# Kernel optimization log

Hardware: AMD Instinct MI355X
Metric: run time of the kernel (lower is better)

Reference implementation:

```python
import jax, jax.numpy as jnp
import numpy as np

N, T, C, K = 32, 1024, 512, 64
EPS = 1e-12  # torch F.normalize eps


def _l2norm(v, axis):
    n = jnp.sqrt(jnp.sum(v * v, axis=axis, keepdims=True))
    return v / jnp.maximum(n, EPS)


def setup_inputs() -> dict:
    key = jax.random.key(0)
    k1, k2 = jax.random.split(key)
    x = jax.random.normal(k1, (N, T, C), dtype=jnp.float32)
    centroids = jax.random.uniform(k2, (K, C), dtype=jnp.float32)
    # mirrors _init_params: conv.weight = 0.2*centroids, conv.bias = -0.1*||centroids||
    W = 0.2 * centroids
    b = -0.1 * jnp.sqrt(jnp.sum(centroids * centroids, axis=1))
    return {"x": x, "W": W, "b": b, "centroids": centroids}


def reference(x, W, b, centroids):
    # x: [N, T, C] -> [N, C, T]
    xt = jnp.transpose(x, (0, 2, 1))
    # 1x1 Conv1d == per-timestep linear: logits [N, K, T]
    logits = jnp.einsum('kc,nct->nkt', W, xt) + b[None, :, None]
    a = jax.nn.softmax(logits, axis=1)  # softmax over clusters
    # vlad[n,k,c] = sum_t a[n,k,t] * (x[n,c,t] - centroid[k,c])
    #            = (a @ x^T) - sum_t(a) * centroid  (GEMM form, same math)
    vlad = jnp.einsum('nkt,nct->nkc', a, xt) - a.sum(axis=-1)[:, :, None] * centroids[None]
    vlad = _l2norm(vlad, axis=2)          # intra-normalization per cluster
    vlad = vlad.reshape(vlad.shape[0], -1)
    vlad = _l2norm(vlad, axis=1)          # global L2 normalization
    return vlad
```

## Files before the change

### kernel.cpp

```cpp
#include <hip/hip_runtime.h>
#include <cmath>

namespace {

constexpr int N = 32, T = 1024, C = 512, K = 64;
constexpr float EPS = 1e-12f;

typedef short s8v __attribute__((ext_vector_type(8)));
typedef short s4v __attribute__((ext_vector_type(4)));
typedef float f4v __attribute__((ext_vector_type(4)));

__device__ inline unsigned short f2bh(float f) {
  __bf16 h = (__bf16)f;
  return __builtin_bit_cast(unsigned short, h);
}
__device__ inline float bh2f(unsigned short u) {
  __bf16 h = __builtin_bit_cast(__bf16, u);
  return (float)h;
}

#define MFMA16(A, B, Cc) __builtin_amdgcn_mfma_f32_16x16x32_bf16((A), (B), (Cc), 0, 0, 0)

__global__ __launch_bounds__(512, 4) void k_gemm1(
    const float* __restrict__ x, const float* __restrict__ W,
    const float* __restrict__ b, float* __restrict__ aT,
    float* __restrict__ asum_part) {
  __shared__ __align__(16) unsigned short sm[4 * 64 * 72];
  __shared__ float asum_l[512];
  unsigned short* xh_s = sm;
  unsigned short* xl_s = sm + 64 * 72;
  unsigned short* wh_s = sm + 2 * 64 * 72;
  unsigned short* wl_s = sm + 3 * 64 * 72;

  const int tid = threadIdx.x;
  const int w = tid >> 6, lane = tid & 63, lm = lane & 15, lq = lane >> 4;
  const int th = w >> 2;
  const int kq = w & 3;
  const long r0 = (long)blockIdx.x * 64;
  const int n = blockIdx.x >> 4, tl = blockIdx.x & 15;

  f4v acc[2] = {};
  float4 px[2], pw[2];
#pragma unroll
  for (int r = 0; r < 2; ++r) {
    const int f = tid + r * 512, t = f >> 4, cg = f & 15;
    px[r] = *(const float4*)&x[(r0 + t) * C + cg * 4];
    pw[r] = *(const float4*)&W[(long)t * C + cg * 4];
  }

  for (int c0 = 0; c0 < C; c0 += 64) {
    __syncthreads();
#pragma unroll
    for (int r = 0; r < 2; ++r) {
      const int f = tid + r * 512, t = f >> 4, cg = f & 15;
      const float ex[4] = {px[r].x, px[r].y, px[r].z, px[r].w};
      const float ew[4] = {pw[r].x, pw[r].y, pw[r].z, pw[r].w};
      s4v xh, xl, wh, wl;
#pragma unroll
      for (int i = 0; i < 4; ++i) {
        unsigned short hb = f2bh(ex[i]);
        xh[i] = (short)hb; xl[i] = (short)f2bh(ex[i] - bh2f(hb));
        hb = f2bh(ew[i]);
        wh[i] = (short)hb; wl[i] = (short)f2bh(ew[i] - bh2f(hb));
      }
      *(s4v*)&xh_s[t * 72 + cg * 4] = xh;
      *(s4v*)&xl_s[t * 72 + cg * 4] = xl;
      *(s4v*)&wh_s[t * 72 + cg * 4] = wh;
      *(s4v*)&wl_s[t * 72 + cg * 4] = wl;
    }
    __syncthreads();
    if (c0 + 64 < C) {
#pragma unroll
      for (int r = 0; r < 2; ++r) {
        const int f = tid + r * 512, t = f >> 4, cg = f & 15;
        px[r] = *(const float4*)&x[(r0 + t) * C + c0 + 64 + cg * 4];
        pw[r] = *(const float4*)&W[(long)t * C + c0 + 64 + cg * 4];
      }
    }

#pragma unroll
    for (int ks = 0; ks < 2; ++ks) {
      const int col = ks * 32 + lq * 8;
      s8v ah[2], al[2];
#pragma unroll
      for (int i = 0; i < 2; ++i) {
        ah[i] = *(const s8v*)&xh_s[(th * 32 + i * 16 + lm) * 72 + col];
        al[i] = *(const s8v*)&xl_s[(th * 32 + i * 16 + lm) * 72 + col];
      }
      const s8v bh = *(const s8v*)&wh_s[(kq * 16 + lm) * 72 + col];
      const s8v bl = *(const s8v*)&wl_s[(kq * 16 + lm) * 72 + col];
#pragma unroll
      for (int i = 0; i < 2; ++i) {
        acc[i] = MFMA16(ah[i], bh, acc[i]);
        acc[i] = MFMA16(ah[i], bl, acc[i]);
        acc[i] = MFMA16(al[i], bh, acc[i]);
      }
    }
  }
  __syncthreads();

  float* Ls = (float*)sm;
  float* Ls2 = (float*)((unsigned char*)sm + 17408);
  const float bias = b[kq * 16 + lm];
#pragma unroll
  for (int i = 0; i < 2; ++i)
#pragma unroll
    for (int r = 0; r < 4; ++r)
      Ls[(th * 32 + i * 16 + lq * 4 + r) * 68 + kq * 16 + lm] =
          acc[i][r] + bias;
  __syncthreads();

  {
    const int row = tid >> 3, q = tid & 7;
    float av[8];
#pragma unroll
    for (int u = 0; u < 2; ++u)
      *(float4*)&av[u * 4] = *(const float4*)&Ls[row * 68 + q * 8 + u * 4];
    float m = av[0];
#pragma unroll
    for (int i = 1; i < 8; ++i) m = fmaxf(m, av[i]);
    m = fmaxf(m, __shfl_xor(m, 1, 64));
    m = fmaxf(m, __shfl_xor(m, 2, 64));
    m = fmaxf(m, __shfl_xor(m, 4, 64));
    float sum = 0.f;
#pragma unroll
    for (int i = 0; i < 8; ++i) {
      av[i] = __expf(av[i] - m);
      sum += av[i];
    }
    sum += __shfl_xor(sum, 1, 64);
    sum += __shfl_xor(sum, 2, 64);
    sum += __shfl_xor(sum, 4, 64);
    const float inv = 1.f / sum;
    float ps[8];
#pragma unroll
    for (int i = 0; i < 8; ++i) {
      av[i] *= inv;
      ps[i] = av[i];
      Ls2[(q * 8 + i) * 68 + row] = av[i];
    }
#pragma unroll
    for (int s = 8; s < 64; s <<= 1)
#pragma unroll
      for (int i = 0; i < 8; ++i) ps[i] += __shfl_xor(ps[i], s, 64);
    if (lane < 8) {
#pragma unroll
      for (int i = 0; i < 8; ++i) asum_l[w * 64 + q * 8 + i] = ps[i];
    }
  }
  __syncthreads();

  if (tid < 64) {
    float s = 0.f;
#pragma unroll
    for (int j = 0; j < 8; ++j) s += asum_l[j * 64 + tid];
    asum_part[(n * 16 + tl) * 64 + tid] = s;
  }
#pragma unroll
  for (int r = 0; r < 2; ++r) {
    const int u = tid + r * 512, k = u >> 4, tg = u & 15;
    *(float4*)&aT[((long)n * K + k) * T + tl * 64 + tg * 4] =
        *(const float4*)&Ls2[k * 68 + tg * 4];
  }
}

__global__ __launch_bounds__(512, 4) void k_gemm2(
    const float* __restrict__ x, const float* __restrict__ aT,
    const float* __restrict__ asum_part, const float* __restrict__ cent,
    float* __restrict__ vlad, float* __restrict__ ssq_part) {
  __shared__ __align__(16) unsigned short sm[(2 * 64 + 2 * 32) * 72];
  __shared__ float asum_l[64];
  __shared__ float ssq_l[128];
  unsigned short* ah_s = sm;
  unsigned short* al_s = sm + 64 * 72;
  unsigned short* xh_s = sm + 2 * 64 * 72;
  unsigned short* xl_s = sm + 2 * 64 * 72 + 32 * 72;

  const int tid = threadIdx.x;
  const int w = tid >> 6, lane = tid & 63, lm = lane & 15, lq = lane >> 4;
  const int kh = w >> 1;
  const int ch = w & 1;
  const int p = blockIdx.x;
  const int g = p >> 3;
  const int n = ((g & 3) << 3) | (p & 7);
  const int cq = g >> 2;
  const int c0 = cq * 32;

  if (tid < 64) {
    float s = 0.f;
#pragma unroll
    for (int tl = 0; tl < 16; ++tl) s += asum_part[(n * 16 + tl) * 64 + tid];
    asum_l[tid] = s;
  }

  f4v acc = {};
  float4 pa[2], px;
#pragma unroll
  for (int r = 0; r < 2; ++r) {
    const int u = tid + r * 512, k = u >> 4, tg = u & 15;
    pa[r] = *(const float4*)&aT[((long)n * K + k) * T + tg * 4];
  }
  {
    const int cg = tid & 7, tq = tid >> 3;
    px = *(const float4*)&x[((long)n * T + tq) * C + c0 + cg * 4];
  }

  for (int t0 = 0; t0 < T; t0 += 64) {
    __syncthreads();
#pragma unroll
    for (int r = 0; r < 2; ++r) {
      const int u = tid + r * 512, k = u >> 4, tg = u & 15;
      const float e[4] = {pa[r].x, pa[r].y, pa[r].z, pa[r].w};
      s4v h, l;
#pragma unroll
      for (int i = 0; i < 4; ++i) {
        unsigned short hb = f2bh(e[i]);
        h[i] = (short)hb;
        l[i] = (short)f2bh(e[i] - bh2f(hb));
      }
      *(s4v*)&ah_s[k * 72 + tg * 4] = h;
      *(s4v*)&al_s[k * 72 + tg * 4] = l;
    }
    {
      const int cg = tid & 7, tq = tid >> 3;
      const float e4[4] = {px.x, px.y, px.z, px.w};
#pragma unroll
      for (int cc = 0; cc < 4; ++cc) {
        const float e = e4[cc];
        const unsigned short hb = f2bh(e);
        xh_s[(cg * 4 + cc) * 72 + tq] = hb;
        xl_s[(cg * 4 + cc) * 72 + tq] = f2bh(e - bh2f(hb));
      }
    }
    __syncthreads();
    if (t0 + 64 < T) {
#pragma unroll
      for (int r = 0; r < 2; ++r) {
        const int u = tid + r * 512, k = u >> 4, tg = u & 15;
        pa[r] = *(const float4*)&aT[((long)n * K + k) * T + t0 + 64 + tg * 4];
      }
      const int cg = tid & 7, tq = tid >> 3;
      px = *(const float4*)&x[((long)n * T + t0 + 64 + tq) * C + c0 + cg * 4];
    }

#pragma unroll
    for (int ks = 0; ks < 2; ++ks) {
      const int col = ks * 32 + lq * 8;
      const s8v ah = *(const s8v*)&ah_s[(kh * 16 + lm) * 72 + col];
      const s8v al = *(const s8v*)&al_s[(kh * 16 + lm) * 72 + col];
      const s8v bh = *(const s8v*)&xh_s[(ch * 16 + lm) * 72 + col];
      const s8v bl = *(const s8v*)&xl_s[(ch * 16 + lm) * 72 + col];
      acc = MFMA16(ah, bh, acc);
      acc = MFMA16(ah, bl, acc);
      acc = MFMA16(al, bh, acc);
    }
  }

  float ssqp[4];
#pragma unroll
  for (int r = 0; r < 4; ++r) {
    const int k = kh * 16 + lq * 4 + r;
    const float as = asum_l[k];
    const int c = c0 + ch * 16 + lm;
    const float v = acc[r] - as * cent[(long)k * C + c];
    vlad[((long)n * K + k) * C + c] = v;
    ssqp[r] = v * v;
  }
#pragma unroll
  for (int r = 0; r < 4; ++r) {
    float s = ssqp[r];
    s += __shfl_xor(s, 1, 64);
    s += __shfl_xor(s, 2, 64);
    s += __shfl_xor(s, 4, 64);
    s += __shfl_xor(s, 8, 64);
    ssqp[r] = s;
  }
  if (lm == 0) {
#pragma unroll
    for (int r = 0; r < 4; ++r)
      ssq_l[(kh * 16 + lq * 4 + r) * 2 + ch] = ssqp[r];
  }
  __syncthreads();
  if (tid < 64)
    ssq_part[(n * 16 + cq) * 64 + tid] = ssq_l[tid * 2] + ssq_l[tid * 2 + 1];
}

__global__ __launch_bounds__(256) void k_norm(
    const float* __restrict__ vlad, const float* __restrict__ ssq_part,
    float* __restrict__ out) {
  __shared__ float denom[64];
  __shared__ float contrib[64];
  __shared__ float ginv;

  const int tid = threadIdx.x;
  const int n = blockIdx.x >> 4;
  const int chunk = blockIdx.x & 15;

  if (tid < 64) {
    float ss = 0.f;
#pragma unroll
    for (int q = 0; q < 16; ++q) ss += ssq_part[(n * 16 + q) * 64 + tid];
    const float d = fmaxf(sqrtf(ss), EPS);
    denom[tid] = d;
    contrib[tid] = ss / (d * d);
  }
  __syncthreads();
  if (tid == 0) {
    float s = 0.f;
#pragma unroll
    for (int k = 0; k < K; ++k) s += contrib[k];
    ginv = 1.0f / fmaxf(sqrtf(s), EPS);
  }
  __syncthreads();

#pragma unroll
  for (int q = 0; q < 2; ++q) {
    const int f4 = tid + q * 256;
    const long off = chunk * 2048 + (long)f4 * 4;
    const int k = (int)(off >> 9);
    float4 v = *(const float4*)&vlad[(long)n * K * C + off];
    const float sc = ginv / denom[k];
    v.x *= sc; v.y *= sc; v.z *= sc; v.w *= sc;
    *(float4*)&out[(long)n * K * C + off] = v;
  }
}

}

extern "C" void kernel_launch(void* const* d_in, const int* in_sizes, int n_in,
                              void* d_out, int out_size, void* d_ws,
                              size_t ws_size, hipStream_t stream) {
  const float* x = reinterpret_cast<const float*>(d_in[0]);
  const float* W = reinterpret_cast<const float*>(d_in[1]);
  const float* b = reinterpret_cast<const float*>(d_in[2]);
  const float* cent = reinterpret_cast<const float*>(d_in[3]);
  float* out = reinterpret_cast<float*>(d_out);

  float* p = reinterpret_cast<float*>(d_ws);
  float* aTg = p;                 p += (size_t)N * K * T;
  float* vlad = p;                p += (size_t)N * K * C;
  float* asum_part = p;           p += (size_t)512 * 64;
  float* ssq_part = p;

  k_gemm1<<<(N * T) / 64, 512, 0, stream>>>(x, W, b, aTg, asum_part);
  k_gemm2<<<N * 16, 512, 0, stream>>>(x, aTg, asum_part, cent, vlad, ssq_part);
  k_norm<<<N * 16, 256, 0, stream>>>(vlad, ssq_part, out);
}
```

Baseline: 130.9 us.

## Retile GEMMs, store softmax as bf16 hi/lo, split-T gemm2, fuse norm

```diff
diff --git a/kernel.cpp b/kernel.cpp
--- a/kernel.cpp
+++ b/kernel.cpp
@@ -8,6 +8,7 @@
 
 typedef short s8v __attribute__((ext_vector_type(8)));
 typedef short s4v __attribute__((ext_vector_type(4)));
+typedef short s2v __attribute__((ext_vector_type(2)));
 typedef float f4v __attribute__((ext_vector_type(4)));
 
 __device__ inline unsigned short f2bh(float f) {
@@ -21,93 +22,101 @@
 
 #define MFMA16(A, B, Cc) __builtin_amdgcn_mfma_f32_16x16x32_bf16((A), (B), (Cc), 0, 0, 0)
 
-__global__ __launch_bounds__(512, 4) void k_gemm1(
+__global__ __launch_bounds__(256, 4) void k_gemm1(
     const float* __restrict__ x, const float* __restrict__ W,
-    const float* __restrict__ b, float* __restrict__ aT,
-    float* __restrict__ asum_part) {
-  __shared__ __align__(16) unsigned short sm[4 * 64 * 72];
-  __shared__ float asum_l[512];
+    const float* __restrict__ b, unsigned short* __restrict__ aTh,
+    unsigned short* __restrict__ aTl, float* __restrict__ asum_part) {
+  __shared__ __align__(16) unsigned short sm[13824];
+  __shared__ float asum_l[256];
   unsigned short* xh_s = sm;
-  unsigned short* xl_s = sm + 64 * 72;
-  unsigned short* wh_s = sm + 2 * 64 * 72;
-  unsigned short* wl_s = sm + 3 * 64 * 72;
+  unsigned short* xl_s = sm + 2304;
+  unsigned short* wh_s = sm + 4608;
+  unsigned short* wl_s = sm + 9216;
 
   const int tid = threadIdx.x;
   const int w = tid >> 6, lane = tid & 63, lm = lane & 15, lq = lane >> 4;
-  const int th = w >> 2;
-  const int kq = w & 3;
-  const long r0 = (long)blockIdx.x * 64;
-  const int n = blockIdx.x >> 4, tl = blockIdx.x & 15;
+  const int th = w >> 1;
+  const int kh = w & 1;
+  const int n = blockIdx.x >> 5, tl = blockIdx.x & 31;
+  const long r0 = (long)blockIdx.x * 32;
 
   f4v acc[2] = {};
-  float4 px[2], pw[2];
-#pragma unroll
-  for (int r = 0; r < 2; ++r) {
-    const int f = tid + r * 512, t = f >> 4, cg = f & 15;
-    px[r] = *(const float4*)&x[(r0 + t) * C + cg * 4];
-    pw[r] = *(const float4*)&W[(long)t * C + cg * 4];
-  }
-
+  float4 px[2], pw[4];
+
+#define G1_LOAD(c0)                                                          \
+  {                                                                          \
+    const int tq = tid >> 4, cg = tid & 15;                                  \
+    _Pragma("unroll") for (int r = 0; r < 2; ++r)                            \
+        px[r] = *(const float4*)&x[(r0 + r * 16 + tq) * C + (c0) + cg * 4];  \
+    _Pragma("unroll") for (int r = 0; r < 4; ++r)                            \
+        pw[r] = *(const float4*)&W[(long)(r * 16 + tq) * C + (c0) + cg * 4]; \
+  }
+
+#define G1_STAGE()                                                           \
+  {                                                                          \
+    const int tq = tid >> 4, cg = tid & 15;                                  \
+    _Pragma("unroll") for (int r = 0; r < 2; ++r) {                          \
+      const int t = r * 16 + tq;                                             \
+      const float e[4] = {px[r].x, px[r].y, px[r].z, px[r].w};               \
+      s4v h, l;                                                              \
+      _Pragma("unroll") for (int i = 0; i < 4; ++i) {                        \
+        unsigned short hb = f2bh(e[i]);                                      \
+        h[i] = (short)hb; l[i] = (short)f2bh(e[i] - bh2f(hb));               \
+      }                                                                      \
+      *(s4v*)&xh_s[t * 72 + cg * 4] = h;                                     \
+      *(s4v*)&xl_s[t * 72 + cg * 4] = l;                                     \
+    }                                                                        \
+    _Pragma("unroll") for (int r = 0; r < 4; ++r) {                          \
+      const int k = r * 16 + tq;                                             \
+      const float e[4] = {pw[r].x, pw[r].y, pw[r].z, pw[r].w};               \
+      s4v h, l;                                                              \
+      _Pragma("unroll") for (int i = 0; i < 4; ++i) {                        \
+        unsigned short hb = f2bh(e[i]);                                      \
+        h[i] = (short)hb; l[i] = (short)f2bh(e[i] - bh2f(hb));               \
+      }                                                                      \
+      *(s4v*)&wh_s[k * 72 + cg * 4] = h;                                     \
+      *(s4v*)&wl_s[k * 72 + cg * 4] = l;                                     \
+    }                                                                        \
+  }
+
+  G1_LOAD(0);
   for (int c0 = 0; c0 < C; c0 += 64) {
+    G1_STAGE();
     __syncthreads();
-#pragma unroll
-    for (int r = 0; r < 2; ++r) {
-      const int f = tid + r * 512, t = f >> 4, cg = f & 15;
-      const float ex[4] = {px[r].x, px[r].y, px[r].z, px[r].w};
-      const float ew[4] = {pw[r].x, pw[r].y, pw[r].z, pw[r].w};
-      s4v xh, xl, wh, wl;
-#pragma unroll
-      for (int i = 0; i < 4; ++i) {
-        unsigned short hb = f2bh(ex[i]);
-        xh[i] = (short)hb; xl[i] = (short)f2bh(ex[i] - bh2f(hb));
-        hb = f2bh(ew[i]);
-        wh[i] = (short)hb; wl[i] = (short)f2bh(ew[i] - bh2f(hb));
-      }
-      *(s4v*)&xh_s[t * 72 + cg * 4] = xh;
-      *(s4v*)&xl_s[t * 72 + cg * 4] = xl;
-      *(s4v*)&wh_s[t * 72 + cg * 4] = wh;
-      *(s4v*)&wl_s[t * 72 + cg * 4] = wl;
-    }
-    __syncthreads();
-    if (c0 + 64 < C) {
-#pragma unroll
-      for (int r = 0; r < 2; ++r) {
-        const int f = tid + r * 512, t = f >> 4, cg = f & 15;
-        px[r] = *(const float4*)&x[(r0 + t) * C + c0 + 64 + cg * 4];
-        pw[r] = *(const float4*)&W[(long)t * C + c0 + 64 + cg * 4];
-      }
-    }
-
+    if (c0 + 64 < C) G1_LOAD(c0 + 64);
 #pragma unroll
     for (int ks = 0; ks < 2; ++ks) {
       const int col = ks * 32 + lq * 8;
-      s8v ah[2], al[2];
-#pragma unroll
-      for (int i = 0; i < 2; ++i) {
-        ah[i] = *(const s8v*)&xh_s[(th * 32 + i * 16 + lm) * 72 + col];
-        al[i] = *(const s8v*)&xl_s[(th * 32 + i * 16 + lm) * 72 + col];
+      const s8v ah = *(const s8v*)&xh_s[(th * 16 + lm) * 72 + col];
+      const s8v al = *(const s8v*)&xl_s[(th * 16 + lm) * 72 + col];
+      s8v bh[2], bl[2];
+#pragma unroll
+      for (int j = 0; j < 2; ++j) {
+        bh[j] = *(const s8v*)&wh_s[(kh * 32 + j * 16 + lm) * 72 + col];
+        bl[j] = *(const s8v*)&wl_s[(kh * 32 + j * 16 + lm) * 72 + col];
       }
-      const s8v bh = *(const s8v*)&wh_s[(kq * 16 + lm) * 72 + col];
-      const s8v bl = *(const s8v*)&wl_s[(kq * 16 + lm) * 72 + col];
-#pragma unroll
-      for (int i = 0; i < 2; ++i) {
-        acc[i] = MFMA16(ah[i], bh, acc[i]);
-        acc[i] = MFMA16(ah[i], bl, acc[i]);
-        acc[i] = MFMA16(al[i], bh, acc[i]);
+#pragma unroll
+      for (int j = 0; j < 2; ++j) {
+        acc[j] = MFMA16(ah, bh[j], acc[j]);
+        acc[j] = MFMA16(ah, bl[j], acc[j]);
+        acc[j] = MFMA16(al, bh[j], acc[j]);
       }
     }
-  }
-  __syncthreads();
+    __syncthreads();
+  }
+#undef G1_LOAD
+#undef G1_STAGE
 
   float* Ls = (float*)sm;
-  float* Ls2 = (float*)((unsigned char*)sm + 17408);
-  const float bias = b[kq * 16 + lm];
-#pragma unroll
-  for (int i = 0; i < 2; ++i)
+  unsigned short* L2h = sm + 4352;
+  unsigned short* L2l = sm + 6912;
+  const float bias[2] = {b[kh * 32 + lm], b[kh * 32 + 16 + lm]};
+#pragma unroll
+  for (int j = 0; j < 2; ++j)
 #pragma unroll
     for (int r = 0; r < 4; ++r)
-      Ls[(th * 32 + i * 16 + lq * 4 + r) * 68 + kq * 16 + lm] =
-          acc[i][r] + bias;
+      Ls[(th * 16 + lq * 4 + r) * 68 + kh * 32 + j * 16 + lm] =
+          acc[j][r] + bias[j];
   __syncthreads();
 
   {
@@ -137,7 +146,9 @@
     for (int i = 0; i < 8; ++i) {
       av[i] *= inv;
       ps[i] = av[i];
-      Ls2[(q * 8 + i) * 68 + row] = av[i];
+      const unsigned short hb = f2bh(av[i]);
+      L2h[(q * 8 + i) * 40 + row] = hb;
+      L2l[(q * 8 + i) * 40 + row] = f2bh(av[i] - bh2f(hb));
     }
 #pragma unroll
     for (int s = 8; s < 64; s <<= 1)
@@ -151,30 +162,28 @@
   __syncthreads();
 
   if (tid < 64) {
-    float s = 0.f;
-#pragma unroll
-    for (int j = 0; j < 8; ++j) s += asum_l[j * 64 + tid];
-    asum_part[(n * 16 + tl) * 64 + tid] = s;
-  }
-#pragma unroll
-  for (int r = 0; r < 2; ++r) {
-    const int u = tid + r * 512, k = u >> 4, tg = u & 15;
-    *(float4*)&aT[((long)n * K + k) * T + tl * 64 + tg * 4] =
-        *(const float4*)&Ls2[k * 68 + tg * 4];
-  }
-}
-
-__global__ __launch_bounds__(512, 4) void k_gemm2(
-    const float* __restrict__ x, const float* __restrict__ aT,
+    asum_part[(n * 32 + tl) * 64 + tid] = asum_l[tid] + asum_l[64 + tid] +
+                                          asum_l[128 + tid] + asum_l[192 + tid];
+  }
+  {
+    const int k = tid >> 2, tg = tid & 3;
+    const long gb = ((long)n * K + k) * T + tl * 32 + tg * 8;
+    *(s8v*)&aTh[gb] = *(const s8v*)&L2h[k * 40 + tg * 8];
+    *(s8v*)&aTl[gb] = *(const s8v*)&L2l[k * 40 + tg * 8];
+  }
+}
+
+__global__ __launch_bounds__(256, 4) void k_gemm2(
+    const float* __restrict__ x, const unsigned short* __restrict__ aTh,
+    const unsigned short* __restrict__ aTl,
     const float* __restrict__ asum_part, const float* __restrict__ cent,
-    float* __restrict__ vlad, float* __restrict__ ssq_part) {
-  __shared__ __align__(16) unsigned short sm[(2 * 64 + 2 * 32) * 72];
+    float* __restrict__ vpart) {
+  __shared__ __align__(16) unsigned short sm[13824];
   __shared__ float asum_l[64];
-  __shared__ float ssq_l[128];
   unsigned short* ah_s = sm;
-  unsigned short* al_s = sm + 64 * 72;
-  unsigned short* xh_s = sm + 2 * 64 * 72;
-  unsigned short* xl_s = sm + 2 * 64 * 72 + 32 * 72;
+  unsigned short* al_s = sm + 4608;
+  unsigned short* xh_s = sm + 9216;
+  unsigned short* xl_s = sm + 11520;
 
   const int tid = threadIdx.x;
   const int w = tid >> 6, lane = tid & 63, lm = lane & 15, lq = lane >> 4;
@@ -183,145 +192,147 @@
   const int p = blockIdx.x;
   const int g = p >> 3;
   const int n = ((g & 3) << 3) | (p & 7);
-  const int cq = g >> 2;
+  const int h = g >> 2;
+  const int cq = h & 15, ts = h >> 4;
   const int c0 = cq * 32;
+  const int t_base = ts * 512;
+  float* vp = vpart + (size_t)ts * N * K * C;
 
   if (tid < 64) {
     float s = 0.f;
 #pragma unroll
-    for (int tl = 0; tl < 16; ++tl) s += asum_part[(n * 16 + tl) * 64 + tid];
+    for (int tl = 0; tl < 16; ++tl)
+      s += asum_part[(n * 32 + ts * 16 + tl) * 64 + tid];
     asum_l[tid] = s;
   }
 
-  f4v acc = {};
-  float4 pa[2], px;
-#pragma unroll
-  for (int r = 0; r < 2; ++r) {
-    const int u = tid + r * 512, k = u >> 4, tg = u & 15;
-    pa[r] = *(const float4*)&aT[((long)n * K + k) * T + tg * 4];
-  }
-  {
-    const int cg = tid & 7, tq = tid >> 3;
-    px = *(const float4*)&x[((long)n * T + tq) * C + c0 + cg * 4];
-  }
-
-  for (int t0 = 0; t0 < T; t0 += 64) {
+  f4v acc[2] = {};
+  const int ak = tid >> 2, atg = tid & 3;
+  s8v pah[2], pal[2];
+  float4 px[2];
+
+#define G2_LOAD(t0)                                                          \
+  {                                                                          \
+    const long ab = ((long)n * K + ak) * T + t_base + (t0) + atg * 16;       \
+    pah[0] = *(const s8v*)&aTh[ab];                                          \
+    pah[1] = *(const s8v*)&aTh[ab + 8];                                      \
+    pal[0] = *(const s8v*)&aTl[ab];                                          \
+    pal[1] = *(const s8v*)&aTl[ab + 8];                                      \
+    const int cg = tid & 7, tq = tid >> 3;                                   \
+    _Pragma("unroll") for (int i = 0; i < 2; ++i)                            \
+        px[i] = *(const float4*)&x[((long)n * T + t_base + (t0) + tq * 2 +   \
+                                    i) * C + c0 + cg * 4];                   \
+  }
+
+#define G2_STAGE()                                                           \
+  {                                                                          \
+    *(s8v*)&ah_s[ak * 72 + atg * 16] = pah[0];                               \
+    *(s8v*)&ah_s[ak * 72 + atg * 16 + 8] = pah[1];                           \
+    *(s8v*)&al_s[ak * 72 + atg * 16] = pal[0];                               \
+    *(s8v*)&al_s[ak * 72 + atg * 16 + 8] = pal[1];                           \
+    const int cg = tid & 7, tq = tid >> 3;                                   \
+    _Pragma("unroll") for (int cc = 0; cc < 4; ++cc) {                       \
+      s2v h, l;                                                              \
+      _Pragma("unroll") for (int i = 0; i < 2; ++i) {                        \
+        const float e = ((const float*)&px[i])[cc];                          \
+        const unsigned short hb = f2bh(e);                                   \
+        h[i] = (short)hb;                                                    \
+        l[i] = (short)f2bh(e - bh2f(hb));                                    \
+      }                                                                      \
+      *(s2v*)&xh_s[(cg * 4 + cc) * 72 + tq * 2] = h;                         \
+      *(s2v*)&xl_s[(cg * 4 + cc) * 72 + tq * 2] = l;                         \
+    }                                                                        \
+  }
+
+  G2_LOAD(0);
+  for (int t0 = 0; t0 < 512; t0 += 64) {
+    G2_STAGE();
     __syncthreads();
-#pragma unroll
-    for (int r = 0; r < 2; ++r) {
-      const int u = tid + r * 512, k = u >> 4, tg = u & 15;
-      const float e[4] = {pa[r].x, pa[r].y, pa[r].z, pa[r].w};
-      s4v h, l;
-#pragma unroll
-      for (int i = 0; i < 4; ++i) {
-        unsigned short hb = f2bh(e[i]);
-        h[i] = (short)hb;
-        l[i] = (short)f2bh(e[i] - bh2f(hb));
-      }
-      *(s4v*)&ah_s[k * 72 + tg * 4] = h;
-      *(s4v*)&al_s[k * 72 + tg * 4] = l;
-    }
-    {
-      const int cg = tid & 7, tq = tid >> 3;
-      const float e4[4] = {px.x, px.y, px.z, px.w};
-#pragma unroll
-      for (int cc = 0; cc < 4; ++cc) {
-        const float e = e4[cc];
-        const unsigned short hb = f2bh(e);
-        xh_s[(cg * 4 + cc) * 72 + tq] = hb;
-        xl_s[(cg * 4 + cc) * 72 + tq] = f2bh(e - bh2f(hb));
-      }
-    }
-    __syncthreads();
-    if (t0 + 64 < T) {
-#pragma unroll
-      for (int r = 0; r < 2; ++r) {
-        const int u = tid + r * 512, k = u >> 4, tg = u & 15;
-        pa[r] = *(const float4*)&aT[((long)n * K + k) * T + t0 + 64 + tg * 4];
-      }
-      const int cg = tid & 7, tq = tid >> 3;
-      px = *(const float4*)&x[((long)n * T + t0 + 64 + tq) * C + c0 + cg * 4];
-    }
-
+    if (t0 + 64 < 512) G2_LOAD(t0 + 64);
 #pragma unroll
     for (int ks = 0; ks < 2; ++ks) {
       const int col = ks * 32 + lq * 8;
-      const s8v ah = *(const s8v*)&ah_s[(kh * 16 + lm) * 72 + col];
-      const s8v al = *(const s8v*)&al_s[(kh * 16 + lm) * 72 + col];
+      s8v ah[2], al[2];
+#pragma unroll
+      for (int i = 0; i < 2; ++i) {
+        ah[i] = *(const s8v*)&ah_s[(kh * 32 + i * 16 + lm) * 72 + col];
+        al[i] = *(const s8v*)&al_s[(kh * 32 + i * 16 + lm) * 72 + col];
+      }
       const s8v bh = *(const s8v*)&xh_s[(ch * 16 + lm) * 72 + col];
       const s8v bl = *(const s8v*)&xl_s[(ch * 16 + lm) * 72 + col];
-      acc = MFMA16(ah, bh, acc);
-      acc = MFMA16(ah, bl, acc);
-      acc = MFMA16(al, bh, acc);
-    }
-  }
-
-  float ssqp[4];
-#pragma unroll
-  for (int r = 0; r < 4; ++r) {
-    const int k = kh * 16 + lq * 4 + r;
-    const float as = asum_l[k];
-    const int c = c0 + ch * 16 + lm;
-    const float v = acc[r] - as * cent[(long)k * C + c];
-    vlad[((long)n * K + k) * C + c] = v;
-    ssqp[r] = v * v;
-  }
-#pragma unroll
-  for (int r = 0; r < 4; ++r) {
-    float s = ssqp[r];
-    s += __shfl_xor(s, 1, 64);
-    s += __shfl_xor(s, 2, 64);
-    s += __shfl_xor(s, 4, 64);
-    s += __shfl_xor(s, 8, 64);
-    ssqp[r] = s;
-  }
-  if (lm == 0) {
-#pragma unroll
-    for (int r = 0; r < 4; ++r)
-      ssq_l[(kh * 16 + lq * 4 + r) * 2 + ch] = ssqp[r];
-  }
-  __syncthreads();
-  if (tid < 64)
-    ssq_part[(n * 16 + cq) * 64 + tid] = ssq_l[tid * 2] + ssq_l[tid * 2 + 1];
-}
-
-__global__ __launch_bounds__(256) void k_norm(
-    const float* __restrict__ vlad, const float* __restrict__ ssq_part,
-    float* __restrict__ out) {
+#pragma unroll
+      for (int i = 0; i < 2; ++i) {
+        acc[i] = MFMA16(ah[i], bh, acc[i]);
+        acc[i] = MFMA16(ah[i], bl, acc[i]);
+        acc[i] = MFMA16(al[i], bh, acc[i]);
+      }
+    }
+    __syncthreads();
+  }
+#undef G2_LOAD
+#undef G2_STAGE
+
+#pragma unroll
+  for (int i = 0; i < 2; ++i) {
+#pragma unroll
+    for (int r = 0; r < 4; ++r) {
+      const int k = kh * 32 + i * 16 + lq * 4 + r;
+      const int c = c0 + ch * 16 + lm;
+      const float v = acc[i][r] - asum_l[k] * cent[(long)k * C + c];
+      vp[((long)n * K + k) * C + c] = v;
+    }
+  }
+}
+
+__global__ __launch_bounds__(1024) void k_norm(
+    const float* __restrict__ vpart, float* __restrict__ out) {
   __shared__ float denom[64];
   __shared__ float contrib[64];
-  __shared__ float ginv;
+  __shared__ float ginv_s;
 
   const int tid = threadIdx.x;
-  const int n = blockIdx.x >> 4;
-  const int chunk = blockIdx.x & 15;
-
-  if (tid < 64) {
-    float ss = 0.f;
-#pragma unroll
-    for (int q = 0; q < 16; ++q) ss += ssq_part[(n * 16 + q) * 64 + tid];
+  const int n = blockIdx.x;
+  const int k = tid >> 4, q = tid & 15;
+  const long base = ((long)n * K + k) * C + q * 4;
+  const float* p0 = vpart + base;
+  const float* p1 = p0 + (size_t)N * K * C;
+
+  float4 v[8];
+#pragma unroll
+  for (int j = 0; j < 8; ++j) v[j] = *(const float4*)&p0[j * 64];
+#pragma unroll
+  for (int j = 0; j < 8; ++j) {
+    const float4 bvec = *(const float4*)&p1[j * 64];
+    v[j].x += bvec.x; v[j].y += bvec.y; v[j].z += bvec.z; v[j].w += bvec.w;
+  }
+  float ss = 0.f;
+#pragma unroll
+  for (int j = 0; j < 8; ++j)
+    ss += v[j].x * v[j].x + v[j].y * v[j].y + v[j].z * v[j].z + v[j].w * v[j].w;
+  ss += __shfl_xor(ss, 1, 64);
+  ss += __shfl_xor(ss, 2, 64);
+  ss += __shfl_xor(ss, 4, 64);
+  ss += __shfl_xor(ss, 8, 64);
+  if (q == 0) {
     const float d = fmaxf(sqrtf(ss), EPS);
-    denom[tid] = d;
-    contrib[tid] = ss / (d * d);
+    denom[k] = d;
+    contrib[k] = ss / (d * d);
   }
   __syncthreads();
   if (tid == 0) {
     float s = 0.f;
 #pragma unroll
-    for (int k = 0; k < K; ++k) s += contrib[k];
-    ginv = 1.0f / fmaxf(sqrtf(s), EPS);
+    for (int kk = 0; kk < K; ++kk) s += contrib[kk];
+    ginv_s = 1.0f / fmaxf(sqrtf(s), EPS);
   }
   __syncthreads();
-
-#pragma unroll
-  for (int q = 0; q < 2; ++q) {
-    const int f4 = tid + q * 256;
-    const long off = chunk * 2048 + (long)f4 * 4;
-    const int k = (int)(off >> 9);
-    float4 v = *(const float4*)&vlad[(long)n * K * C + off];
-    const float sc = ginv / denom[k];
-    v.x *= sc; v.y *= sc; v.z *= sc; v.w *= sc;
-    *(float4*)&out[(long)n * K * C + off] = v;
+  const float sc = ginv_s / denom[k];
+  float* po = out + base;
+#pragma unroll
+  for (int j = 0; j < 8; ++j) {
+    float4 o = v[j];
+    o.x *= sc; o.y *= sc; o.z *= sc; o.w *= sc;
+    *(float4*)&po[j * 64] = o;
   }
 }
 
@@ -336,13 +347,16 @@
   const float* cent = reinterpret_cast<const float*>(d_in[3]);
   float* out = reinterpret_cast<float*>(d_out);
 
-  float* p = reinterpret_cast<float*>(d_ws);
-  float* aTg = p;                 p += (size_t)N * K * T;
-  float* vlad = p;                p += (size_t)N * K * C;
-  float* asum_part = p;           p += (size_t)512 * 64;
-  float* ssq_part = p;
-
-  k_gemm1<<<(N * T) / 64, 512, 0, stream>>>(x, W, b, aTg, asum_part);
-  k_gemm2<<<N * 16, 512, 0, stream>>>(x, aTg, asum_part, cent, vlad, ssq_part);
-  k_norm<<<N * 16, 256, 0, stream>>>(vlad, ssq_part, out);
-}
+  char* pp = reinterpret_cast<char*>(d_ws);
+  unsigned short* aTh = reinterpret_cast<unsigned short*>(pp);
+  pp += (size_t)N * K * T * sizeof(unsigned short);
+  unsigned short* aTl = reinterpret_cast<unsigned short*>(pp);
+  pp += (size_t)N * K * T * sizeof(unsigned short);
+  float* vpart = reinterpret_cast<float*>(pp);
+  pp += (size_t)2 * N * K * C * sizeof(float);
+  float* asum_part = reinterpret_cast<float*>(pp);
+
+  k_gemm1<<<(N * T) / 32, 256, 0, stream>>>(x, W, b, aTh, aTl, asum_part);
+  k_gemm2<<<N * 16 * 2, 256, 0, stream>>>(x, aTh, aTl, asum_part, cent, vpart);
+  k_norm<<<N, 1024, 0, stream>>>(vpart, out);
+}
```

Measured after the change: 130.6 us. Within noise of the previous version (-0.2%).
